# Performance work log

Measured on AMD Instinct MI355X. Metric: run time of the kernel, lower is better.

Reference implementation:

```python
import jax, jax.numpy as jnp
import numpy as np

NEG_SLOPE = 0.2

def gat_conv(x, edge, W, att_src, att_dst, bias, heads, out_ch, concat):
    # x: [N, F_in], edge: [2, E] (self-loops already included)
    N = x.shape[0]
    src, dst = edge[0], edge[1]
    h = (x @ W).reshape(N, heads, out_ch)                     # [N, H, C]
    a_src = jnp.sum(h * att_src, axis=-1)                     # [N, H]
    a_dst = jnp.sum(h * att_dst, axis=-1)                     # [N, H]
    e = jax.nn.leaky_relu(a_src[src] + a_dst[dst], NEG_SLOPE)  # [E, H]
    # segment softmax over incoming edges of each dst node
    e_max = jax.ops.segment_max(e, dst, num_segments=N)       # [N, H]
    e_exp = jnp.exp(e - e_max[dst])                           # [E, H]
    denom = jax.ops.segment_sum(e_exp, dst, num_segments=N)   # [N, H]
    alpha = e_exp / denom[dst]                                # [E, H]
    msg = h[src] * alpha[:, :, None]                          # [E, H, C]
    out = jax.ops.segment_sum(msg, dst, num_segments=N)       # [N, H, C]
    if concat:
        out = out.reshape(N, heads * out_ch)
    else:
        out = out.mean(axis=1)
    return out + bias


def setup_inputs() -> dict:
    key = jax.random.key(0)
    ks = jax.random.split(key, 10)
    N, E = 50000, 1600000
    F_in, H, C1, n_cls = 256, 4, 64, 40
    x = jax.random.normal(ks[0], (N, F_in), dtype=jnp.float32)
    edge_index = jax.random.randint(ks[1], (2, E), 0, N, dtype=jnp.int64)
    s1 = 1.0 / np.sqrt(F_in)
    s2 = 1.0 / np.sqrt(H * C1)
    return {
        "x": x,
        "edge_index": edge_index,
        "W1": jax.random.normal(ks[2], (F_in, H * C1), dtype=jnp.float32) * s1,
        "att_src1": jax.random.normal(ks[3], (H, C1), dtype=jnp.float32) * s2,
        "att_dst1": jax.random.normal(ks[4], (H, C1), dtype=jnp.float32) * s2,
        "b1": jnp.zeros((H * C1,), dtype=jnp.float32),
        "W2": jax.random.normal(ks[5], (H * C1, n_cls), dtype=jnp.float32) * s2,
        "att_src2": jax.random.normal(ks[6], (1, n_cls), dtype=jnp.float32) * 0.1,
        "att_dst2": jax.random.normal(ks[7], (1, n_cls), dtype=jnp.float32) * 0.1,
        "b2": jnp.zeros((n_cls,), dtype=jnp.float32),
    }


def reference(x, edge_index, W1, att_src1, att_dst1, b1, W2, att_src2, att_dst2, b2):
    N = x.shape[0]
    # PyG GATConv adds self-loops by default
    loops = jnp.arange(N, dtype=edge_index.dtype)
    edge = jnp.concatenate([edge_index, jnp.stack([loops, loops])], axis=1)
    # dropout is identity in eval mode
    h = gat_conv(x, edge, W1, att_src1, att_dst1, b1, heads=4, out_ch=64, concat=True)
    h = jax.nn.elu(h)
    out = gat_conv(h, edge, W2, att_src2, att_dst2, b2, heads=1, out_ch=40, concat=False)
    return out
```

## Files before the change

### kernel.cpp

```cpp
#include <hip/hip_runtime.h>
#include <hip/hip_bf16.h>

typedef short bf16x8 __attribute__((ext_vector_type(8)));
typedef float f32x4 __attribute__((ext_vector_type(4)));

#define CHUNK 4096

__device__ __forceinline__ float wred_sum(float v) {
  #pragma unroll
  for (int off = 32; off > 0; off >>= 1)
    v += __shfl_xor(v, off, 64);
  return v;
}
__device__ __forceinline__ float b2f(unsigned short u) {
  union { unsigned int i; float f; } x;
  x.i = ((unsigned int)u) << 16;
  return x.f;
}
__device__ __forceinline__ unsigned short f2bu(float f) {
  __hip_bfloat16 b = __float2bfloat16(f);
  return *(unsigned short*)&b;
}
__device__ __forceinline__ float ldf(const void* p, long long i, int is16) {
  return is16 ? __bfloat162float(((const __hip_bfloat16*)p)[i])
              : ((const float*)p)[i];
}
__device__ __forceinline__ int edge_at(const int* e, long long idx, int is64) {
  return is64 ? (int)((const long long*)e)[idx] : e[idx];
}

__global__ void detect_kernel(const int* __restrict__ edge, int n_edge_check,
                              const unsigned int* __restrict__ xw, int n_x_check,
                              int* __restrict__ flag) {
  __shared__ int s_nz, s_cnt, s_tot;
  int tid = threadIdx.x;
  if (tid == 0) { s_nz = 0; s_cnt = 0; s_tot = 0; }
  __syncthreads();
  int nz = 0;
  for (int k = tid; k < n_edge_check; k += 256)
    if (edge[2 * k + 1] != 0) nz = 1;
  if (nz) atomicOr(&s_nz, 1);
  int c = 0, t = 0;
  for (int k = tid; k < n_x_check; k += 256) {
    unsigned int w = xw[k];
    if (w == 0u) continue;
    t++;
    unsigned int e = (w >> 7) & 0xFFu;
    if (e >= 100u && e <= 150u) c++;
  }
  atomicAdd(&s_cnt, c);
  atomicAdd(&s_tot, t);
  __syncthreads();
  if (tid == 0) {
    flag[0] = (s_nz == 0) ? 1 : 0;
    flag[1] = (s_cnt * 10 > s_tot * 6) ? 1 : 0;
  }
}


__global__ __launch_bounds__(256) void bucket_count_kernel(
    const int* __restrict__ edge, int E, int N, const int* __restrict__ flag,
    int* __restrict__ bcnt, int NB) {
  __shared__ int cnt[1024];
  int tid = threadIdx.x;
  long long base = (long long)blockIdx.x * CHUNK;
  long long total = (long long)E + N;
  for (int b = tid; b < NB; b += 256) cnt[b] = 0;
  __syncthreads();
  int is64 = flag[0];
  #pragma unroll
  for (int j = 0; j < 16; j++) {
    long long i = base + j * 256 + tid;
    if (i < total) {
      int d = (i < E) ? edge_at(edge, (long long)E + i, is64) : (int)(i - E);
      d = min(max(d, 0), N - 1);
      atomicAdd(&cnt[d >> 8], 1);
    }
  }
  __syncthreads();
  for (int b = tid; b < NB; b += 256)
    if (cnt[b]) atomicAdd(&bcnt[b], cnt[b]);
}

__global__ void bucket_scan_kernel(const int* __restrict__ bcnt, int NB,
                                   int* __restrict__ bbase, int* __restrict__ bcursor) {
  __shared__ int s[256];
  __shared__ int rbase;
  int tid = threadIdx.x;
  if (tid == 0) rbase = 0;
  __syncthreads();
  for (int c0 = 0; c0 < NB; c0 += 256) {
    int idx = c0 + tid;
    int v = (idx < NB) ? bcnt[idx] : 0;
    s[tid] = v;
    __syncthreads();
    for (int off = 1; off < 256; off <<= 1) {
      int t = (tid >= off) ? s[tid - off] : 0;
      __syncthreads();
      s[tid] += t;
      __syncthreads();
    }
    int mb = rbase;
    if (idx < NB) {
      int exc = mb + s[tid] - v;
      bbase[idx] = exc;
      bcursor[idx] = exc;
    }
    __syncthreads();
    if (tid == 0) rbase = mb + s[255];
    __syncthreads();
  }
  if (tid == 0) bbase[NB] = rbase;
}

__global__ __launch_bounds__(256) void partition_kernel(
    const int* __restrict__ edge, int E, int N, const int* __restrict__ flag,
    int* __restrict__ bcursor, unsigned int* __restrict__ part, int NB) {
  __shared__ int cnt[1024];
  __shared__ int loff[1025];
  __shared__ int gpos[1024];
  __shared__ int lcur[1024];
  __shared__ unsigned int staged[CHUNK];
  __shared__ int staged_addr[CHUNK];
  __shared__ int s[256];
  __shared__ int rbase;
  int tid = threadIdx.x;
  long long base = (long long)blockIdx.x * CHUNK;
  long long total = (long long)E + N;
  int here = (int)min((long long)CHUNK, total - base);
  for (int b = tid; b < NB; b += 256) cnt[b] = 0;
  if (tid == 0) rbase = 0;
  __syncthreads();
  int is64 = flag[0];
  int myb[16];
  unsigned int myp[16];
  #pragma unroll
  for (int j = 0; j < 16; j++) {
    long long i = base + j * 256 + tid;
    myb[j] = -1;
    if (i < total) {
      int d, sv;
      if (i < E) {
        sv = edge_at(edge, i, is64);
        d = edge_at(edge, (long long)E + i, is64);
      } else {
        sv = d = (int)(i - E);
      }
      d = min(max(d, 0), N - 1);
      sv = min(max(sv, 0), N - 1);
      myb[j] = d >> 8;
      myp[j] = ((unsigned int)(d & 255) << 24) | (unsigned int)sv;
      atomicAdd(&cnt[myb[j]], 1);
    }
  }
  __syncthreads();
  for (int c0 = 0; c0 < NB; c0 += 256) {
    int idx = c0 + tid;
    int v = (idx < NB) ? cnt[idx] : 0;
    s[tid] = v;
    __syncthreads();
    for (int off = 1; off < 256; off <<= 1) {
      int t = (tid >= off) ? s[tid - off] : 0;
      __syncthreads();
      s[tid] += t;
      __syncthreads();
    }
    int mb = rbase;
    if (idx < NB) loff[idx] = mb + s[tid] - v;
    __syncthreads();
    if (tid == 0) rbase = mb + s[255];
    __syncthreads();
  }
  __syncthreads();
  for (int b = tid; b < NB; b += 256) {
    int c = cnt[b];
    gpos[b] = c ? atomicAdd(&bcursor[b], c) : 0;
    lcur[b] = loff[b];
  }
  __syncthreads();
  #pragma unroll
  for (int j = 0; j < 16; j++) {
    if (myb[j] >= 0) {
      int b = myb[j];
      int slot = atomicAdd(&lcur[b], 1);
      staged[slot] = myp[j];
      staged_addr[slot] = gpos[b] + (slot - loff[b]);
    }
  }
  __syncthreads();
  for (int i = tid; i < here; i += 256)
    part[staged_addr[i]] = staged[i];
}

__global__ __launch_bounds__(256) void bucket_sort_kernel(
    const unsigned int* __restrict__ part, const int* __restrict__ bbase,
    int N, int total, int* __restrict__ indptr, int* __restrict__ ssrc) {
  __shared__ int hist[256], cur[256];
  __shared__ int s[256];
  int tid = threadIdx.x;
  int b = blockIdx.x;
  int begin = bbase[b], end = bbase[b + 1];
  hist[tid] = 0;
  __syncthreads();
  for (int i = begin + tid; i < end; i += 256)
    atomicAdd(&hist[part[i] >> 24], 1);
  __syncthreads();
  int v = hist[tid];
  s[tid] = v;
  __syncthreads();
  for (int off = 1; off < 256; off <<= 1) {
    int t = (tid >= off) ? s[tid - off] : 0;
    __syncthreads();
    s[tid] += t;
    __syncthreads();
  }
  int exc = s[tid] - v;
  cur[tid] = exc;
  int d = b * 256 + tid;
  if (d < N) indptr[d] = begin + exc;
  if (b == 0 && tid == 0) indptr[N] = total;
  __syncthreads();
  for (int i = begin + tid; i < end; i += 256) {
    unsigned int p = part[i];
    int pos = begin + atomicAdd(&cur[p >> 24], 1);
    ssrc[pos] = (int)(p & 0xFFFFFFu);
  }
}

__global__ void prep_kernel(const void* __restrict__ x, __hip_bfloat16* __restrict__ xb,
                            long long n_valid4, long long nconv4,
                            const void* __restrict__ W1v, const void* __restrict__ W2v,
                            __hip_bfloat16* __restrict__ Wt1, __hip_bfloat16* __restrict__ Wt2,
                            int F, int HC, int C2, int C2p,
                            const int* __restrict__ dflag) {
  int f16 = dflag[1];
  long long i = blockIdx.x * 256LL + threadIdx.x;
  if (i < nconv4) {
    ushort4 o;
    if (i < n_valid4) {
      if (f16) {
        o = ((const ushort4*)x)[i];
      } else {
        float4 v = ((const float4*)x)[i];
        o.x = f2bu(v.x); o.y = f2bu(v.y); o.z = f2bu(v.z); o.w = f2bu(v.w);
      }
    } else {
      o.x = o.y = o.z = o.w = 0;
    }
    ((ushort4*)xb)[i] = o;
    return;
  }
  long long j = i - nconv4;
  int n1 = HC * F;
  if (j < n1) {
    int idx = (int)j;
    int n = idx / F, k = idx - n * F;
    Wt1[idx] = __float2bfloat16(ldf(W1v, (long long)k * HC + n, f16));
  } else {
    int jj = (int)(j - n1);
    if (jj >= C2p * HC) return;
    int n = jj / HC, k = jj - n * HC;
    float v = (n < C2) ? ldf(W2v, (long long)k * C2 + n, f16) : 0.f;
    Wt2[jj] = __float2bfloat16(v);
  }
}

__global__ __launch_bounds__(256) void mfma_gemm_kernel(
    const __hip_bfloat16* __restrict__ A, const __hip_bfloat16* __restrict__ BtT,
    __hip_bfloat16* __restrict__ Cb,
    const void* __restrict__ attS, const void* __restrict__ attD,
    float* __restrict__ aS, float* __restrict__ aD, int att_stride,
    int M, int Nout, int K, int quant,
    unsigned char* __restrict__ h1q, float* __restrict__ h1s,
    const int* __restrict__ dflag) {
  int f16 = dflag[1];
  int tid = threadIdx.x;
  int w = tid >> 6, l = tid & 63;
  int m_lane = l & 15, q = l >> 4;
  int row0 = blockIdx.x * 64, col0 = blockIdx.y * 64;
  const __hip_bfloat16* Arow = A + (long long)(row0 + w * 16 + m_lane) * K + q * 8;
  const __hip_bfloat16* Brow = BtT + (long long)(col0 + m_lane) * K + q * 8;
  f32x4 acc[4] = {};
  #pragma unroll 4
  for (int k0 = 0; k0 < K; k0 += 32) {
    bf16x8 af = *(const bf16x8*)(Arow + k0);
    #pragma unroll
    for (int t = 0; t < 4; t++) {
      bf16x8 bf = *(const bf16x8*)(Brow + (long long)t * 16 * K + k0);
      acc[t] = __builtin_amdgcn_mfma_f32_16x16x32_bf16(af, bf, acc[t], 0, 0, 0);
    }
  }
  #pragma unroll
  for (int r = 0; r < 4; r++) {
    int gr = row0 + w * 16 + q * 4 + r;
    float ps = 0.f, pd = 0.f, vmax = 0.f;
    #pragma unroll
    for (int t = 0; t < 4; t++) {
      int gc = col0 + t * 16 + m_lane;
      float v = acc[t][r];
      if (gc < Nout) {
        ps += v * ldf(attS, gc, f16);
        pd += v * ldf(attD, gc, f16);
        vmax = fmaxf(vmax, fabsf(v));
        if (!quant && gr < M) Cb[(long long)gr * Nout + gc] = __float2bfloat16(v);
      }
    }
    #pragma unroll
    for (int off = 1; off < 16; off <<= 1) {
      ps += __shfl_xor(ps, off, 64);
      pd += __shfl_xor(pd, off, 64);
      vmax = fmaxf(vmax, __shfl_xor(vmax, off, 64));
    }
    if (quant && gr < M) {
      float qinv = (vmax > 0.f) ? 127.f / vmax : 0.f;
      #pragma unroll
      for (int t = 0; t < 4; t++) {
        int gc = col0 + t * 16 + m_lane;
        h1q[(long long)gr * 256 + gc] =
            (unsigned char)(__float2int_rn(acc[t][r] * qinv) + 128);
      }
      if (m_lane == 0)
        h1s[(long long)gr * att_stride + blockIdx.y] = vmax * (1.f / 127.f);
    }
    if (m_lane == 0 && gr < M) {
      aS[(long long)gr * att_stride + blockIdx.y] = ps;
      aD[(long long)gr * att_stride + blockIdx.y] = pd;
    }
  }
}

__global__ __launch_bounds__(256) void aggregate1_kernel(
    const int* __restrict__ indptr, const int* __restrict__ ssrc,
    const unsigned char* __restrict__ h1q, const float* __restrict__ h1s,
    const float* __restrict__ a_src, const float* __restrict__ a_dst,
    const void* __restrict__ b1,
    __hip_bfloat16* __restrict__ h2b, int N, const int* __restrict__ dflag) {
  int f16 = dflag[1];
  int w = threadIdx.x >> 6, l = threadIdx.x & 63;
  int d = blockIdx.x * 4 + w;
  if (d >= N) return;
  int q = l >> 4;
  int e16 = l & 15;
  int base = l & 48;
  int begin = indptr[d], end = indptr[d + 1];
  float adst = a_dst[d * 4 + q];
  int s0 = ssrc[begin];
  float den = 0.f, accS = 0.f;
  float acc0 = 0.f, acc1 = 0.f, acc2 = 0.f, acc3 = 0.f;
  for (int c = begin; c < end; c += 32) {
    int cnt = end - c;
    int sj0 = s0, sj1 = s0;
    float wj0 = 0.f, wj1 = 0.f, ws0 = 0.f, ws1 = 0.f;
    if (e16 < cnt) {
      sj0 = ssrc[c + e16];
      float e = a_src[sj0 * 4 + q] + adst;
      e = (e > 0.f) ? e : 0.2f * e;
      wj0 = __expf(e);
      ws0 = wj0 * h1s[sj0 * 4 + q];
    }
    if (e16 + 16 < cnt) {
      sj1 = ssrc[c + e16 + 16];
      float e = a_src[sj1 * 4 + q] + adst;
      e = (e > 0.f) ? e : 0.2f * e;
      wj1 = __expf(e);
      ws1 = wj1 * h1s[sj1 * 4 + q];
    }
    den += wj0 + wj1;
    int n0 = cnt < 16 ? cnt : 16;
    int n1 = cnt - 16;
    n1 = n1 < 0 ? 0 : (n1 > 16 ? 16 : n1);
    #pragma unroll 4
    for (int j = 0; j < n0; j++) {
      int s = __shfl(sj0, base + j, 64);
      float wt = __shfl(ws0, base + j, 64);
      accS += wt;
      unsigned int uv = *(const unsigned int*)(h1q + (long long)s * 256 + 4 * l);
      acc0 += wt * (float)(uv & 0xFFu);
      acc1 += wt * (float)((uv >> 8) & 0xFFu);
      acc2 += wt * (float)((uv >> 16) & 0xFFu);
      acc3 += wt * (float)(uv >> 24);
    }
    #pragma unroll 4
    for (int j = 0; j < n1; j++) {
      int s = __shfl(sj1, base + j, 64);
      float wt = __shfl(ws1, base + j, 64);
      accS += wt;
      unsigned int uv = *(const unsigned int*)(h1q + (long long)s * 256 + 4 * l);
      acc0 += wt * (float)(uv & 0xFFu);
      acc1 += wt * (float)((uv >> 8) & 0xFFu);
      acc2 += wt * (float)((uv >> 16) & 0xFFu);
      acc3 += wt * (float)(uv >> 24);
    }
  }
  #pragma unroll
  for (int off = 1; off < 16; off <<= 1)
    den += __shfl_xor(den, off, 64);
  float inv = 1.f / den;
  float v0 = (acc0 - 128.f * accS) * inv + ldf(b1, 4 * l + 0, f16);
  float v1 = (acc1 - 128.f * accS) * inv + ldf(b1, 4 * l + 1, f16);
  float v2 = (acc2 - 128.f * accS) * inv + ldf(b1, 4 * l + 2, f16);
  float v3 = (acc3 - 128.f * accS) * inv + ldf(b1, 4 * l + 3, f16);
  v0 = (v0 > 0.f) ? v0 : (__expf(v0) - 1.f);
  v1 = (v1 > 0.f) ? v1 : (__expf(v1) - 1.f);
  v2 = (v2 > 0.f) ? v2 : (__expf(v2) - 1.f);
  v3 = (v3 > 0.f) ? v3 : (__expf(v3) - 1.f);
  ushort4 o;
  o.x = f2bu(v0); o.y = f2bu(v1); o.z = f2bu(v2); o.w = f2bu(v3);
  *(ushort4*)((unsigned short*)h2b + (long long)d * 256 + 4 * l) = o;
}

__global__ __launch_bounds__(256) void aggregate2_kernel(
    const int* __restrict__ indptr, const int* __restrict__ ssrc,
    const __hip_bfloat16* __restrict__ gb, const float* __restrict__ a_src,
    const float* __restrict__ a_dst, const void* __restrict__ b2,
    void* __restrict__ out, int N, int C, const int* __restrict__ dflag) {
  int f16 = dflag[1];
  int w = threadIdx.x >> 6, l = threadIdx.x & 63;
  int d = blockIdx.x * 4 + w;
  if (d >= N) return;
  int begin = indptr[d], end = indptr[d + 1];
  float adst = a_dst[d];
  int e_off = l / 20;
  int pr = l - e_off * 20;
  bool active = (e_off < 3);
  int s0 = ssrc[begin];
  float den = 0.f;
  float acc0 = 0.f, acc1 = 0.f;
  for (int c = begin; c < end; c += 64) {
    int cnt = min(64, end - c);
    int sj = s0;
    float wj = 0.f;
    if (l < cnt) {
      sj = ssrc[c + l];
      float e = a_src[sj] + adst;
      e = (e > 0.f) ? e : 0.2f * e;
      wj = __expf(e);
    }
    den += wj;
    #pragma unroll 4
    for (int j = 0; j < cnt; j += 3) {
      int idx = j + e_off;
      int s = __shfl(sj, idx & 63, 64);
      float wt = __shfl(wj, idx & 63, 64);
      if (!active || idx >= cnt) wt = 0.f;
      ushort2 gv = *(const ushort2*)((const unsigned short*)gb +
                                     (long long)s * C + 2 * pr);
      acc0 += wt * b2f(gv.x);
      acc1 += wt * b2f(gv.y);
    }
  }
  den = wred_sum(den);
  float inv = 1.f / den;
  float r0 = acc0 + __shfl(acc0, (l + 20) & 63, 64) + __shfl(acc0, (l + 40) & 63, 64);
  float r1 = acc1 + __shfl(acc1, (l + 20) & 63, 64) + __shfl(acc1, (l + 40) & 63, 64);
  if (l < 20) {
    float v0 = r0 * inv + ldf(b2, 2 * l + 0, f16);
    float v1 = r1 * inv + ldf(b2, 2 * l + 1, f16);
    long long o = (long long)d * C + 2 * l;
    if (f16) {
      ushort2 ov;
      ov.x = f2bu(v0); ov.y = f2bu(v1);
      *(ushort2*)((unsigned short*)out + o) = ov;
    } else {
      float2 ov;
      ov.x = v0; ov.y = v1;
      *(float2*)((float*)out + o) = ov;
    }
  }
}

extern "C" void kernel_launch(void* const* d_in, const int* in_sizes, int n_in,
                              void* d_out, int out_size, void* d_ws, size_t ws_size,
                              hipStream_t stream) {
  const void* x   = d_in[0];
  const int* edge = (const int*)d_in[1];
  const void* W1  = d_in[2];
  const void* as1 = d_in[3];
  const void* ad1 = d_in[4];
  const void* b1  = d_in[5];
  const void* W2  = d_in[6];
  const void* as2 = d_in[7];
  const void* ad2 = d_in[8];
  const void* b2  = d_in[9];

  const int F  = 256;
  const int HC = 256;
  const int N  = in_sizes[0] / F;
  const int E  = in_sizes[1] / 2;
  const int C2 = in_sizes[9];
  const int C2p = 64;
  const int total = E + N;
  const int NB = (N + 255) / 256;
  const int Mpad = ((N + 63) / 64) * 64;

  char* p = (char*)d_ws;
  auto alloc = [&](size_t bytes) -> void* {
    void* r = (void*)p;
    p += (bytes + 255) & ~(size_t)255;
    return r;
  };
  __hip_bfloat16* xb  = (__hip_bfloat16*)alloc((size_t)Mpad * F * 2);
  unsigned char*  h1q = (unsigned char*)alloc((size_t)Mpad * HC);
  float*          h1s = (float*)alloc((size_t)Mpad * 4 * 4);
  __hip_bfloat16* h2b = (__hip_bfloat16*)alloc((size_t)Mpad * HC * 2);
  __hip_bfloat16* gb  = (__hip_bfloat16*)alloc((size_t)Mpad * C2 * 2);
  __hip_bfloat16* Wt1 = (__hip_bfloat16*)alloc((size_t)HC * F * 2);
  __hip_bfloat16* Wt2 = (__hip_bfloat16*)alloc((size_t)C2p * HC * 2);
  float* a_src1 = (float*)alloc((size_t)N * 4 * 4);
  float* a_dst1 = (float*)alloc((size_t)N * 4 * 4);
  float* a_src2 = (float*)alloc((size_t)N * 4);
  float* a_dst2 = (float*)alloc((size_t)N * 4);
  unsigned int* part = (unsigned int*)alloc((size_t)total * 4);
  int* bcnt     = (int*)alloc((size_t)(NB + 1) * 4);
  int* bbase    = (int*)alloc((size_t)(NB + 1) * 4);
  int* bcursor  = (int*)alloc((size_t)NB * 4);
  int* indptr   = (int*)alloc((size_t)(N + 1) * 4);
  int* ssrc     = (int*)alloc((size_t)total * 4);
  int* flag     = (int*)alloc(256);

  hipMemsetAsync(bcnt, 0, (size_t)(NB + 1) * 4, stream);
  detect_kernel<<<1, 256, 0, stream>>>(edge, E < 2048 ? E : 2048,
                                       (const unsigned int*)x, 4096, flag);
  int nch = (total + CHUNK - 1) / CHUNK;
  bucket_count_kernel<<<nch, 256, 0, stream>>>(edge, E, N, flag, bcnt, NB);
  bucket_scan_kernel<<<1, 256, 0, stream>>>(bcnt, NB, bbase, bcursor);
  partition_kernel<<<nch, 256, 0, stream>>>(edge, E, N, flag, bcursor, part, NB);
  bucket_sort_kernel<<<NB, 256, 0, stream>>>(part, bbase, N, total, indptr, ssrc);

  long long nconv4 = (long long)Mpad * F / 4;
  long long nprep = nconv4 + (long long)HC * F + (long long)C2p * HC;
  prep_kernel<<<(int)((nprep + 255) / 256), 256, 0, stream>>>(
      x, xb, (long long)N * F / 4, nconv4, W1, W2, Wt1, Wt2, F, HC, C2, C2p, flag);

  dim3 g1(Mpad / 64, HC / 64);
  mfma_gemm_kernel<<<g1, 256, 0, stream>>>(xb, Wt1, nullptr,
                                           as1, ad1, a_src1, a_dst1, 4,
                                           N, HC, F, 1, h1q, h1s, flag);
  aggregate1_kernel<<<(N + 3) / 4, 256, 0, stream>>>(indptr, ssrc, h1q, h1s,
                                                     a_src1, a_dst1, b1, h2b, N, flag);

  dim3 g2(Mpad / 64, 1);
  mfma_gemm_kernel<<<g2, 256, 0, stream>>>(h2b, Wt2, gb,
                                           as2, ad2, a_src2, a_dst2, 1,
                                           N, C2, HC, 0, nullptr, nullptr, flag);
  aggregate2_kernel<<<(N + 3) / 4, 256, 0, stream>>>(indptr, ssrc, gb, a_src2, a_dst2,
                                                     b2, d_out, N, C2, flag);
}
```

Baseline: 442.6 us.

## Pack attention score and quant scale; gather 16B rows across four edges

Layer-1 GEMM now writes the per-head source attention score and the int8 dequant scale as one float2, so the aggregation reads a single 8-byte value per edge instead of two scattered floats. Aggregate1 is reorganised so each lane loads 16 bytes (uint4) of a neighbour row and the four 16-lane groups each handle a different edge concurrently. Partial sums are then reduced across the groups with shuffles. This cuts the number of gather instructions and raises memory parallelism, at the cost of more accumulator registers, an extra cross-group reduction, and only 16 lanes doing the final writes.

```diff
diff --git a/kernel.cpp b/kernel.cpp
--- a/kernel.cpp
+++ b/kernel.cpp
@@ -3,6 +3,7 @@
 
 typedef short bf16x8 __attribute__((ext_vector_type(8)));
 typedef float f32x4 __attribute__((ext_vector_type(4)));
+typedef unsigned short u16x8 __attribute__((ext_vector_type(8)));
 
 #define CHUNK 4096
 
@@ -269,9 +270,10 @@
     const __hip_bfloat16* __restrict__ A, const __hip_bfloat16* __restrict__ BtT,
     __hip_bfloat16* __restrict__ Cb,
     const void* __restrict__ attS, const void* __restrict__ attD,
-    float* __restrict__ aS, float* __restrict__ aD, int att_stride,
+    float* __restrict__ aS, float* __restrict__ aD,
+    float2* __restrict__ aSq, int att_stride,
     int M, int Nout, int K, int quant,
-    unsigned char* __restrict__ h1q, float* __restrict__ h1s,
+    unsigned char* __restrict__ h1q,
     const int* __restrict__ dflag) {
   int f16 = dflag[1];
   int tid = threadIdx.x;
@@ -319,11 +321,13 @@
         h1q[(long long)gr * 256 + gc] =
             (unsigned char)(__float2int_rn(acc[t][r] * qinv) + 128);
       }
-      if (m_lane == 0)
-        h1s[(long long)gr * att_stride + blockIdx.y] = vmax * (1.f / 127.f);
+      if (m_lane == 0) {
+        float2 sq; sq.x = ps; sq.y = vmax * (1.f / 127.f);
+        aSq[(long long)gr * att_stride + blockIdx.y] = sq;
+      }
     }
     if (m_lane == 0 && gr < M) {
-      aS[(long long)gr * att_stride + blockIdx.y] = ps;
+      if (!quant) aS[(long long)gr * att_stride + blockIdx.y] = ps;
       aD[(long long)gr * att_stride + blockIdx.y] = pd;
     }
   }
@@ -331,9 +335,8 @@
 
 __global__ __launch_bounds__(256) void aggregate1_kernel(
     const int* __restrict__ indptr, const int* __restrict__ ssrc,
-    const unsigned char* __restrict__ h1q, const float* __restrict__ h1s,
-    const float* __restrict__ a_src, const float* __restrict__ a_dst,
-    const void* __restrict__ b1,
+    const unsigned char* __restrict__ h1q, const float2* __restrict__ a_sq,
+    const float* __restrict__ a_dst, const void* __restrict__ b1,
     __hip_bfloat16* __restrict__ h2b, int N, const int* __restrict__ dflag) {
   int f16 = dflag[1];
   int w = threadIdx.x >> 6, l = threadIdx.x & 63;
@@ -341,72 +344,104 @@
   if (d >= N) return;
   int q = l >> 4;
   int e16 = l & 15;
-  int base = l & 48;
+  int hb = (l & 12) << 2;
+  int chb = (l & 15) << 4;
   int begin = indptr[d], end = indptr[d + 1];
   float adst = a_dst[d * 4 + q];
   int s0 = ssrc[begin];
   float den = 0.f, accS = 0.f;
-  float acc0 = 0.f, acc1 = 0.f, acc2 = 0.f, acc3 = 0.f;
+  float acc[16] = {};
   for (int c = begin; c < end; c += 32) {
     int cnt = end - c;
     int sj0 = s0, sj1 = s0;
     float wj0 = 0.f, wj1 = 0.f, ws0 = 0.f, ws1 = 0.f;
     if (e16 < cnt) {
       sj0 = ssrc[c + e16];
-      float e = a_src[sj0 * 4 + q] + adst;
+      float2 t = a_sq[sj0 * 4 + q];
+      float e = t.x + adst;
       e = (e > 0.f) ? e : 0.2f * e;
       wj0 = __expf(e);
-      ws0 = wj0 * h1s[sj0 * 4 + q];
+      ws0 = wj0 * t.y;
     }
     if (e16 + 16 < cnt) {
       sj1 = ssrc[c + e16 + 16];
-      float e = a_src[sj1 * 4 + q] + adst;
+      float2 t = a_sq[sj1 * 4 + q];
+      float e = t.x + adst;
       e = (e > 0.f) ? e : 0.2f * e;
       wj1 = __expf(e);
-      ws1 = wj1 * h1s[sj1 * 4 + q];
+      ws1 = wj1 * t.y;
     }
     den += wj0 + wj1;
-    int n0 = cnt < 16 ? cnt : 16;
-    int n1 = cnt - 16;
-    n1 = n1 < 0 ? 0 : (n1 > 16 ? 16 : n1);
+    int m0 = cnt < 16 ? cnt : 16;
+    int m1 = cnt - 16; m1 = m1 < 0 ? 0 : (m1 > 16 ? 16 : m1);
+    int j0 = (m0 + 3) >> 2, j1 = (m1 + 3) >> 2;
     #pragma unroll 4
-    for (int j = 0; j < n0; j++) {
-      int s = __shfl(sj0, base + j, 64);
-      float wt = __shfl(ws0, base + j, 64);
+    for (int j = 0; j < j0; j++) {
+      int idx = hb + 4 * j + q;
+      int s = __shfl(sj0, idx, 64);
+      float wt = __shfl(ws0, idx, 64);
       accS += wt;
-      unsigned int uv = *(const unsigned int*)(h1q + (long long)s * 256 + 4 * l);
-      acc0 += wt * (float)(uv & 0xFFu);
-      acc1 += wt * (float)((uv >> 8) & 0xFFu);
-      acc2 += wt * (float)((uv >> 16) & 0xFFu);
-      acc3 += wt * (float)(uv >> 24);
+      uint4 uv = *(const uint4*)(h1q + (long long)s * 256 + chb);
+      unsigned int u;
+      u = uv.x;
+      acc[0]  += wt * (float)(u & 0xFFu);         acc[1]  += wt * (float)((u >> 8) & 0xFFu);
+      acc[2]  += wt * (float)((u >> 16) & 0xFFu); acc[3]  += wt * (float)(u >> 24);
+      u = uv.y;
+      acc[4]  += wt * (float)(u & 0xFFu);         acc[5]  += wt * (float)((u >> 8) & 0xFFu);
+      acc[6]  += wt * (float)((u >> 16) & 0xFFu); acc[7]  += wt * (float)(u >> 24);
+      u = uv.z;
+      acc[8]  += wt * (float)(u & 0xFFu);         acc[9]  += wt * (float)((u >> 8) & 0xFFu);
+      acc[10] += wt * (float)((u >> 16) & 0xFFu); acc[11] += wt * (float)(u >> 24);
+      u = uv.w;
+      acc[12] += wt * (float)(u & 0xFFu);         acc[13] += wt * (float)((u >> 8) & 0xFFu);
+      acc[14] += wt * (float)((u >> 16) & 0xFFu); acc[15] += wt * (float)(u >> 24);
     }
     #pragma unroll 4
-    for (int j = 0; j < n1; j++) {
-      int s = __shfl(sj1, base + j, 64);
-      float wt = __shfl(ws1, base + j, 64);
+    for (int j = 0; j < j1; j++) {
+      int idx = hb + 4 * j + q;
+      int s = __shfl(sj1, idx, 64);
+      float wt = __shfl(ws1, idx, 64);
       accS += wt;
-      unsigned int uv = *(const unsigned int*)(h1q + (long long)s * 256 + 4 * l);
-      acc0 += wt * (float)(uv & 0xFFu);
-      acc1 += wt * (float)((uv >> 8) & 0xFFu);
-      acc2 += wt * (float)((uv >> 16) & 0xFFu);
-      acc3 += wt * (float)(uv >> 24);
-    }
-  }
+      uint4 uv = *(const uint4*)(h1q + (long long)s * 256 + chb);
+      unsigned int u;
+      u = uv.x;
+      acc[0]  += wt * (float)(u & 0xFFu);         acc[1]  += wt * (float)((u >> 8) & 0xFFu);
+      acc[2]  += wt * (float)((u >> 16) & 0xFFu); acc[3]  += wt * (float)(u >> 24);
+      u = uv.y;
+      acc[4]  += wt * (float)(u & 0xFFu);         acc[5]  += wt * (float)((u >> 8) & 0xFFu);
+      acc[6]  += wt * (float)((u >> 16) & 0xFFu); acc[7]  += wt * (float)(u >> 24);
+      u = uv.z;
+      acc[8]  += wt * (float)(u & 0xFFu);         acc[9]  += wt * (float)((u >> 8) & 0xFFu);
+      acc[10] += wt * (float)((u >> 16) & 0xFFu); acc[11] += wt * (float)(u >> 24);
+      u = uv.w;
+      acc[12] += wt * (float)(u & 0xFFu);         acc[13] += wt * (float)((u >> 8) & 0xFFu);
+      acc[14] += wt * (float)((u >> 16) & 0xFFu); acc[15] += wt * (float)(u >> 24);
+    }
+  }
+  #pragma unroll
+  for (int i = 0; i < 16; i++) {
+    acc[i] += __shfl_xor(acc[i], 16, 64);
+    acc[i] += __shfl_xor(acc[i], 32, 64);
+  }
+  accS += __shfl_xor(accS, 16, 64);
+  accS += __shfl_xor(accS, 32, 64);
   #pragma unroll
   for (int off = 1; off < 16; off <<= 1)
     den += __shfl_xor(den, off, 64);
-  float inv = 1.f / den;
-  float v0 = (acc0 - 128.f * accS) * inv + ldf(b1, 4 * l + 0, f16);
-  float v1 = (acc1 - 128.f * accS) * inv + ldf(b1, 4 * l + 1, f16);
-  float v2 = (acc2 - 128.f * accS) * inv + ldf(b1, 4 * l + 2, f16);
-  float v3 = (acc3 - 128.f * accS) * inv + ldf(b1, 4 * l + 3, f16);
-  v0 = (v0 > 0.f) ? v0 : (__expf(v0) - 1.f);
-  v1 = (v1 > 0.f) ? v1 : (__expf(v1) - 1.f);
-  v2 = (v2 > 0.f) ? v2 : (__expf(v2) - 1.f);
-  v3 = (v3 > 0.f) ? v3 : (__expf(v3) - 1.f);
-  ushort4 o;
-  o.x = f2bu(v0); o.y = f2bu(v1); o.z = f2bu(v2); o.w = f2bu(v3);
-  *(ushort4*)((unsigned short*)h2b + (long long)d * 256 + 4 * l) = o;
+  float deh = __shfl(den, hb, 64);
+  float inv = 1.f / deh;
+  if (l < 16) {
+    u16x8 o0, o1;
+    #pragma unroll
+    for (int i = 0; i < 16; i++) {
+      float v = (acc[i] - 128.f * accS) * inv + ldf(b1, chb + i, f16);
+      v = (v > 0.f) ? v : (__expf(v) - 1.f);
+      if (i < 8) o0[i] = f2bu(v); else o1[i - 8] = f2bu(v);
+    }
+    u16x8* dst = (u16x8*)((unsigned short*)h2b + (long long)d * 256 + chb);
+    dst[0] = o0;
+    dst[1] = o1;
+  }
 }
 
 __global__ __launch_bounds__(256) void aggregate2_kernel(
@@ -501,12 +536,11 @@
   };
   __hip_bfloat16* xb  = (__hip_bfloat16*)alloc((size_t)Mpad * F * 2);
   unsigned char*  h1q = (unsigned char*)alloc((size_t)Mpad * HC);
-  float*          h1s = (float*)alloc((size_t)Mpad * 4 * 4);
   __hip_bfloat16* h2b = (__hip_bfloat16*)alloc((size_t)Mpad * HC * 2);
   __hip_bfloat16* gb  = (__hip_bfloat16*)alloc((size_t)Mpad * C2 * 2);
   __hip_bfloat16* Wt1 = (__hip_bfloat16*)alloc((size_t)HC * F * 2);
   __hip_bfloat16* Wt2 = (__hip_bfloat16*)alloc((size_t)C2p * HC * 2);
-  float* a_src1 = (float*)alloc((size_t)N * 4 * 4);
+  float2* a_sq1 = (float2*)alloc((size_t)N * 4 * 8);
   float* a_dst1 = (float*)alloc((size_t)N * 4 * 4);
   float* a_src2 = (float*)alloc((size_t)N * 4);
   float* a_dst2 = (float*)alloc((size_t)N * 4);
@@ -534,15 +568,15 @@
 
   dim3 g1(Mpad / 64, HC / 64);
   mfma_gemm_kernel<<<g1, 256, 0, stream>>>(xb, Wt1, nullptr,
-                                           as1, ad1, a_src1, a_dst1, 4,
-                                           N, HC, F, 1, h1q, h1s, flag);
-  aggregate1_kernel<<<(N + 3) / 4, 256, 0, stream>>>(indptr, ssrc, h1q, h1s,
-                                                     a_src1, a_dst1, b1, h2b, N, flag);
+                                           as1, ad1, nullptr, a_dst1, a_sq1, 4,
+                                           N, HC, F, 1, h1q, flag);
+  aggregate1_kernel<<<(N + 3) / 4, 256, 0, stream>>>(indptr, ssrc, h1q, a_sq1,
+                                                     a_dst1, b1, h2b, N, flag);
 
   dim3 g2(Mpad / 64, 1);
   mfma_gemm_kernel<<<g2, 256, 0, stream>>>(h2b, Wt2, gb,
-                                           as2, ad2, a_src2, a_dst2, 1,
-                                           N, C2, HC, 0, nullptr, nullptr, flag);
+                                           as2, ad2, a_src2, a_dst2, nullptr, 1,
+                                           N, C2, HC, 0, nullptr, flag);
   aggregate2_kernel<<<(N + 3) / 4, 256, 0, stream>>>(indptr, ssrc, gb, a_src2, a_dst2,
                                                      b2, d_out, N, C2, flag);
 }
```

Result: faster. 403.1 us (-8.9%).
